# Kernel optimization log

Hardware: AMD Instinct MI355X
Metric: run time of the kernel (lower is better)

## Reference

```python
import jax, jax.numpy as jnp
import numpy as np

B_, L_, D_ = 8, 2048, 1024      # batch, seq_len, d_model
E, DS, K = 2, 16, 4             # expand, d_state, d_conv
DI = E * D_                     # d_inner = 2048
DTR = (D_ + 15) // 16           # dt_rank = 64


def setup_inputs() -> dict:
    key = jax.random.key(0)
    ks = jax.random.split(key, 8)
    g = lambda k, sh, sc=0.02: jax.random.normal(k, sh, jnp.float32) * sc
    return {
        "x": jax.random.normal(ks[0], (B_, L_, D_), jnp.float32),
        "ln_w": jnp.ones((D_,), jnp.float32),
        "ln_b": jnp.zeros((D_,), jnp.float32),
        "W_in": g(ks[1], (D_, 2 * DI)),
        "conv_w": g(ks[2], (DI, 1, K), 0.1),
        "conv_b": jnp.zeros((DI,), jnp.float32),
        "W_x": g(ks[3], (DI, DTR + 2 * DS)),
        "W_dt": g(ks[4], (DTR, DI), 0.1),
        "b_dt": jnp.full((DI,), -4.0, jnp.float32),  # softplus(-4) ~ 0.018 (small init dt)
        "A_log": jnp.log(jnp.broadcast_to(jnp.arange(1, DS + 1, dtype=jnp.float32), (DI, DS))),
        "Dp": jnp.ones((DI,), jnp.float32),
        "W_out": g(ks[5], (DI, D_)),
    }


def _mamba_block(x, ln_w, ln_b, W_in, conv_w, conv_b, W_x, W_dt, b_dt, A_log, Dp, W_out):
    # pre-norm
    mu = jnp.mean(x, axis=-1, keepdims=True)
    var = jnp.var(x, axis=-1, keepdims=True)
    xn = (x - mu) / jnp.sqrt(var + 1e-5) * ln_w + ln_b

    # input projection -> (u, z), each (B, L, DI)
    xz = jnp.einsum('bld,de->ble', xn, W_in)
    u, z = jnp.split(xz, 2, axis=-1)

    # causal depthwise conv1d along L
    uc = jax.lax.conv_general_dilated(
        u.transpose(0, 2, 1), conv_w, window_strides=(1,), padding=[(K - 1, 0)],
        feature_group_count=DI, dimension_numbers=('NCH', 'OIH', 'NCH'))
    u = jax.nn.silu(uc.transpose(0, 2, 1) + conv_b)

    # input-dependent SSM params
    xd = jnp.einsum('bld,de->ble', u, W_x)          # (B, L, DTR + 2*DS)
    dt = jax.nn.softplus(jnp.einsum('blr,rd->bld', xd[..., :DTR], W_dt) + b_dt)  # (B, L, DI)
    Bm = xd[..., DTR:DTR + DS]                       # (B, L, DS)
    Cm = xd[..., DTR + DS:]                          # (B, L, DS)
    A = -jnp.exp(A_log)                              # (DI, DS)

    # selective scan over time; carry h: (B, DI, DS)
    def step(h, inp):
        dt_t, u_t, B_t, C_t = inp                    # (B,DI),(B,DI),(B,DS),(B,DS)
        dA = jnp.exp(dt_t[..., None] * A)            # (B, DI, DS)
        h = h * dA + (dt_t * u_t)[..., None] * B_t[:, None, :]
        y = jnp.einsum('bds,bs->bd', h, C_t)
        return h, y

    h0 = jnp.zeros((x.shape[0], DI, DS), x.dtype)
    xs = (dt.transpose(1, 0, 2), u.transpose(1, 0, 2), Bm.transpose(1, 0, 2), Cm.transpose(1, 0, 2))
    _, ys = jax.lax.scan(step, h0, xs)               # ys: (L, B, DI)

    y = ys.transpose(1, 0, 2) + u * Dp
    y = y * jax.nn.silu(z)
    # output projection + residual (dropout is identity in eval)
    return jnp.einsum('bld,de->ble', y, W_out) + x


def reference(x, ln_w, ln_b, W_in, conv_w, conv_b, W_x, W_dt, b_dt, A_log, Dp, W_out):
    return _mamba_block(x, ln_w, ln_b, W_in, conv_w, conv_b, W_x, W_dt, b_dt, A_log, Dp, W_out)
```

## Files before the change

### kernel.cpp

```cpp
#include <hip/hip_runtime.h>

#define NB 8
#define NL 2048
#define ND 1024
#define NDI 2048
#define NDS 16
#define NDTR 64
#define NM (NB * NL)
#define CH 16
#define CL (NL / CH)

__device__ __forceinline__ float bf2f(unsigned int u) {
  union { unsigned int i; float f; } c; c.i = u << 16; return c.f;
}
__device__ __forceinline__ float lo16(unsigned int w) { return __uint_as_float(w << 16); }
__device__ __forceinline__ float hi16(unsigned int w) { return __uint_as_float(w & 0xffff0000u); }
__device__ __forceinline__ unsigned short f2bf(float f) {
  unsigned int x = __float_as_uint(f);
  x = x + 0x7fffu + ((x >> 16) & 1u);
  return (unsigned short)(x >> 16);
}
__device__ __forceinline__ void dec8(int4 raw, float* f) {
  f[0] = lo16((unsigned)raw.x); f[1] = hi16((unsigned)raw.x);
  f[2] = lo16((unsigned)raw.y); f[3] = hi16((unsigned)raw.y);
  f[4] = lo16((unsigned)raw.z); f[5] = hi16((unsigned)raw.z);
  f[6] = lo16((unsigned)raw.w); f[7] = hi16((unsigned)raw.w);
}
__device__ __forceinline__ float softplus_fast(float x) {
  return fmaxf(x, 0.f) + __logf(1.f + __expf(-fabsf(x)));
}

typedef __bf16 bf16x8 __attribute__((ext_vector_type(8)));
typedef float f32x4 __attribute__((ext_vector_type(4)));

__device__ __forceinline__ void gld_lds16(const unsigned short* g, unsigned short* l) {
  __builtin_amdgcn_global_load_lds(
      (const __attribute__((address_space(1))) unsigned int*)g,
      (__attribute__((address_space(3))) unsigned int*)l, 16, 0, 0);
}

__global__ __launch_bounds__(256) void k_ln(const float* __restrict__ x,
    const float* __restrict__ lw, const float* __restrict__ lb,
    unsigned short* __restrict__ xn)
{
  const int row = blockIdx.x;
  const int tid = threadIdx.x;
  const float* xr = x + (size_t)row * ND;
  float4 v = reinterpret_cast<const float4*>(xr)[tid];
  float s  = v.x + v.y + v.z + v.w;
  float s2 = v.x*v.x + v.y*v.y + v.z*v.z + v.w*v.w;
  #pragma unroll
  for (int m = 32; m >= 1; m >>= 1) {
    s  += __shfl_xor(s, m);
    s2 += __shfl_xor(s2, m);
  }
  __shared__ float red[8];
  const int wid = tid >> 6;
  if ((tid & 63) == 0) { red[wid] = s; red[4 + wid] = s2; }
  __syncthreads();
  s  = red[0] + red[1] + red[2] + red[3];
  s2 = red[4] + red[5] + red[6] + red[7];
  const float mu   = s * (1.0f / ND);
  const float var  = s2 * (1.0f / ND) - mu * mu;
  const float rstd = rsqrtf(var + 1e-5f);
  const float4 wv = reinterpret_cast<const float4*>(lw)[tid];
  const float4 bv = reinterpret_cast<const float4*>(lb)[tid];
  ushort4 o;
  o.x = f2bf((v.x - mu) * rstd * wv.x + bv.x);
  o.y = f2bf((v.y - mu) * rstd * wv.y + bv.y);
  o.z = f2bf((v.z - mu) * rstd * wv.z + bv.z);
  o.w = f2bf((v.w - mu) * rstd * wv.w + bv.w);
  reinterpret_cast<ushort4*>(xn + (size_t)row * ND)[tid] = o;
}

__global__ __launch_bounds__(256) void k_transpose(
    const float* __restrict__ W, unsigned short* __restrict__ WT,
    const int K, const int N)
{
  __shared__ float t[32][33];
  const int k0 = blockIdx.y * 32, n0 = blockIdx.x * 32;
  const int tx = threadIdx.x & 31, ty = threadIdx.x >> 5;
  #pragma unroll
  for (int r = 0; r < 4; ++r)
    t[ty + r * 8][tx] = W[(size_t)(k0 + ty + r * 8) * N + n0 + tx];
  __syncthreads();
  #pragma unroll
  for (int r = 0; r < 4; ++r)
    WT[(size_t)(n0 + ty + r * 8) * K + k0 + tx] = f2bf(t[tx][ty + r * 8]);
}

template<int MODE>
__global__ __launch_bounds__(512, 4) void k_mfma3(
    const unsigned short* __restrict__ A, const unsigned short* __restrict__ BT,
    const int K, const int N, void* __restrict__ O0, void* __restrict__ O1,
    const float* __restrict__ aux)
{
  __shared__ __align__(16) unsigned short sh[24576];
  const int tid = threadIdx.x, lane = tid & 63, wv = tid >> 6;
  const int wm = wv >> 2, wn = wv & 3;
  const int m16 = lane & 15, kb = lane >> 4;
  const int swzs = (((kb * 16) ^ (((m16 >> 1) & 3) << 4)) >> 1);
  const int arow = wm * 64 + m16;
  const int brow = wn * 64 + m16;

  int wg = blockIdx.x;
  const int cpx = gridDim.x >> 3;
  wg = (wg & 7) * cpx + (wg >> 3);
  const int gnx = N >> 8;
  const int m0 = (wg / gnx) << 7;
  const int n0 = (wg % gnx) << 8;

  f32x4 acc[4][4];
  #pragma unroll
  for (int i = 0; i < 4; ++i)
    #pragma unroll
    for (int j = 0; j < 4; ++j)
      #pragma unroll
      for (int r = 0; r < 4; ++r) acc[i][j][r] = 0.f;

  auto STAGE_A = [&](int kg, unsigned short* base) {
    const int s = wv * 64 + lane;
    const int row = s >> 2;
    const int c = (s & 3) ^ ((row >> 1) & 3);
    gld_lds16(A + (size_t)(m0 + row) * K + kg + c * 8, base + wv * 512);
  };
  auto STAGE_B = [&](int kg, unsigned short* base) {
    #pragma unroll
    for (int jj = 0; jj < 2; ++jj) {
      const int s = (wv * 2 + jj) * 64 + lane;
      const int row = s >> 2;
      const int c = (s & 3) ^ ((row >> 1) & 3);
      gld_lds16(BT + (size_t)(n0 + row) * K + kg + c * 8, base + (wv * 2 + jj) * 512);
    }
  };

  STAGE_A(0, sh);
  STAGE_B(0, sh + 4096);
  asm volatile("s_waitcnt vmcnt(0)" ::: "memory");
  __builtin_amdgcn_s_barrier();

  const int NT = K >> 5;
  for (int t = 0; t < NT; ++t) {
    const int buf = t & 1;
    const unsigned short* cA = sh + buf * 12288;
    const unsigned short* cB = cA + 4096;
    unsigned short* nBuf = sh + (buf ^ 1) * 12288;
    const bool more = (t + 1 < NT);
    if (more) {
      const int kn = (t + 1) << 5;
      STAGE_A(kn, nBuf);
      STAGE_B(kn, nBuf + 4096);
    }
    bf16x8 aF[4], bF[4];
    #pragma unroll
    for (int i = 0; i < 4; ++i)
      aF[i] = *reinterpret_cast<const bf16x8*>(cA + (arow + i * 16) * 32 + swzs);
    #pragma unroll
    for (int j = 0; j < 4; ++j)
      bF[j] = *reinterpret_cast<const bf16x8*>(cB + (brow + j * 16) * 32 + swzs);
    __builtin_amdgcn_sched_barrier(0);
    __builtin_amdgcn_s_setprio(1);
    #pragma unroll
    for (int i = 0; i < 4; ++i)
      #pragma unroll
      for (int j = 0; j < 4; ++j)
        acc[i][j] = __builtin_amdgcn_mfma_f32_16x16x32_bf16(aF[i], bF[j], acc[i][j], 0, 0, 0);
    __builtin_amdgcn_s_setprio(0);
    if (more) asm volatile("s_waitcnt vmcnt(0)" ::: "memory");
    __builtin_amdgcn_s_barrier();
  }

  {
    float* fsh = (float*)sh;
    constexpr int LDP = 260;
    const int erow = tid >> 4;
    const int ec0  = tid & 15;
    #pragma unroll
    for (int i = 0; i < 4; ++i) {
      __builtin_amdgcn_s_barrier();
      #pragma unroll
      for (int j = 0; j < 4; ++j)
        #pragma unroll
        for (int r = 0; r < 4; ++r)
          fsh[(wm * 16 + kb * 4 + r) * LDP + wn * 64 + j * 16 + m16] = acc[i][j][r];
      __builtin_amdgcn_s_barrier();
      const int grow = m0 + (erow >> 4) * 64 + i * 16 + (erow & 15);
      #pragma unroll
      for (int q = 0; q < 4; ++q) {
        const int c = (ec0 + q * 16) * 4;
        float4 v = *reinterpret_cast<const float4*>(&fsh[erow * LDP + c]);
        const int colg = n0 + c;
        if constexpr (MODE == 0) {
          ushort4 o = {f2bf(v.x), f2bf(v.y), f2bf(v.z), f2bf(v.w)};
          unsigned short* dst = (colg < NDI)
              ? (unsigned short*)O0 + (size_t)grow * NDI + colg
              : (unsigned short*)O1 + (size_t)grow * NDI + colg - NDI;
          *reinterpret_cast<ushort4*>(dst) = o;
        } else {
          float4 rv = *reinterpret_cast<const float4*>(aux + (size_t)grow * N + colg);
          float4 o = {v.x + rv.x, v.y + rv.y, v.z + rv.z, v.w + rv.w};
          *reinterpret_cast<float4*>((float*)O0 + (size_t)grow * N + colg) = o;
        }
      }
    }
  }
  (void)O1; (void)aux;
}

__global__ __launch_bounds__(256) void k_mfma_dt(
    const unsigned short* __restrict__ A, const unsigned short* __restrict__ BT,
    const int K, void* __restrict__ O0, const float* __restrict__ aux, const int N)
{
  __shared__ __align__(16) unsigned short As[128 * 32];
  __shared__ __align__(16) unsigned short Bs[128 * 32];
  __shared__ __align__(16) float fshd[32 * 132];
  const int tid = threadIdx.x;
  const int lane = tid & 63;
  const int wv = tid >> 6;
  const int wm = wv >> 1, wn = wv & 1;
  const int m0 = blockIdx.y * 128, n0 = blockIdx.x * 128;
  const int m16 = lane & 15, kb = lane >> 4;
  const int wbase = wv * 64;

  f32x4 acc[4][4];
  #pragma unroll
  for (int i = 0; i < 4; ++i)
    #pragma unroll
    for (int j = 0; j < 4; ++j)
      #pragma unroll
      for (int r = 0; r < 4; ++r) acc[i][j][r] = 0.f;

  for (int k0 = 0; k0 < K; k0 += 32) {
    #pragma unroll
    for (int it = 0; it < 2; ++it) {
      const int c = it * 256 + tid;
      const int r = c >> 2, cb = c & 3;
      gld_lds16(A  + (size_t)(m0 + r) * K + k0 + cb * 8, As + (size_t)(it * 256 + wbase) * 8);
      gld_lds16(BT + (size_t)(n0 + r) * K + k0 + cb * 8, Bs + (size_t)(it * 256 + wbase) * 8);
    }
    __syncthreads();
    bf16x8 af[4], bfr[4];
    #pragma unroll
    for (int i = 0; i < 4; ++i)
      af[i] = *reinterpret_cast<const bf16x8*>(&As[(wm * 64 + i * 16 + m16) * 32 + kb * 8]);
    #pragma unroll
    for (int j = 0; j < 4; ++j)
      bfr[j] = *reinterpret_cast<const bf16x8*>(&Bs[(wn * 64 + j * 16 + m16) * 32 + kb * 8]);
    #pragma unroll
    for (int i = 0; i < 4; ++i)
      #pragma unroll
      for (int j = 0; j < 4; ++j)
        acc[i][j] = __builtin_amdgcn_mfma_f32_16x16x32_bf16(af[i], bfr[j], acc[i][j], 0, 0, 0);
    __syncthreads();
  }

  {
    constexpr int LDP = 132;
    const int erow = tid >> 3;
    const int ec0  = tid & 7;
    #pragma unroll
    for (int i = 0; i < 4; ++i) {
      __syncthreads();
      #pragma unroll
      for (int j = 0; j < 4; ++j)
        #pragma unroll
        for (int r = 0; r < 4; ++r)
          fshd[(wm * 16 + kb * 4 + r) * LDP + wn * 64 + j * 16 + m16] = acc[i][j][r];
      __syncthreads();
      const int grow = m0 + (erow >> 4) * 64 + i * 16 + (erow & 15);
      #pragma unroll
      for (int q = 0; q < 4; ++q) {
        const int c = (ec0 + q * 8) * 4;
        float4 v = *reinterpret_cast<const float4*>(&fshd[erow * LDP + c]);
        const int colg = n0 + c;
        ushort4 o;
        o.x = f2bf(softplus_fast(v.x + aux[colg + 0]));
        o.y = f2bf(softplus_fast(v.y + aux[colg + 1]));
        o.z = f2bf(softplus_fast(v.z + aux[colg + 2]));
        o.w = f2bf(softplus_fast(v.w + aux[colg + 3]));
        *reinterpret_cast<ushort4*>((unsigned short*)O0 + (size_t)grow * N + colg) = o;
      }
    }
  }
}

__global__ __launch_bounds__(256) void k_conv(
    const unsigned short* __restrict__ up, const float* __restrict__ cw,
    const float* __restrict__ cb, unsigned short* __restrict__ u)
{
  const int tid = threadIdx.x;
  const int c0 = tid * 8;
  const int lt = blockIdx.x & 127;
  const int b  = blockIdx.x >> 7;
  const int l0 = lt * 16;

  float4 wv[8];
  #pragma unroll
  for (int j = 0; j < 8; ++j)
    wv[j] = reinterpret_cast<const float4*>(cw + (size_t)c0 * 4)[j];
  float bias[8];
  {
    float4 b0 = reinterpret_cast<const float4*>(cb + c0)[0];
    float4 b1 = reinterpret_cast<const float4*>(cb + c0)[1];
    bias[0]=b0.x; bias[1]=b0.y; bias[2]=b0.z; bias[3]=b0.w;
    bias[4]=b1.x; bias[5]=b1.y; bias[6]=b1.z; bias[7]=b1.w;
  }

  const size_t base = ((size_t)b * NL + l0) * NDI + c0;
  float w0[8], w1[8], w2[8];
  if (l0 >= 3) {
    int4 r0 = *reinterpret_cast<const int4*>(up + base - 3 * NDI);
    int4 r1 = *reinterpret_cast<const int4*>(up + base - 2 * NDI);
    int4 r2 = *reinterpret_cast<const int4*>(up + base - 1 * NDI);
    dec8(r0, w0); dec8(r1, w1); dec8(r2, w2);
  } else {
    #pragma unroll
    for (int j = 0; j < 8; ++j) { w0[j] = 0.f; w1[j] = 0.f; w2[j] = 0.f; }
  }

  #pragma unroll
  for (int l = 0; l < 16; ++l) {
    int4 raw = *reinterpret_cast<const int4*>(up + base + (size_t)l * NDI);
    float cur[8];
    dec8(raw, cur);
    unsigned short o[8];
    #pragma unroll
    for (int j = 0; j < 8; ++j) {
      const float a = bias[j] + wv[j].x * w0[j] + wv[j].y * w1[j]
                              + wv[j].z * w2[j] + wv[j].w * cur[j];
      o[j] = f2bf(a / (1.f + __expf(-a)));
    }
    ushort4 o0 = {o[0], o[1], o[2], o[3]};
    ushort4 o1 = {o[4], o[5], o[6], o[7]};
    unsigned short* dst = u + base + (size_t)l * NDI;
    *reinterpret_cast<ushort4*>(dst)     = o0;
    *reinterpret_cast<ushort4*>(dst + 4) = o1;
    #pragma unroll
    for (int j = 0; j < 8; ++j) { w0[j] = w1[j]; w1[j] = w2[j]; w2[j] = cur[j]; }
  }
}

__global__ __launch_bounds__(256) void k_xd_mfma(
    const unsigned short* __restrict__ A, const unsigned short* __restrict__ BT,
    unsigned short* __restrict__ xdt, float* __restrict__ xb,
    float* __restrict__ xc)
{
  __shared__ __align__(16) unsigned short As[2][64 * 32];
  __shared__ __align__(16) unsigned short Bs[2][96 * 32];
  const int tid = threadIdx.x, lane = tid & 63, wvv = tid >> 6;
  const int m0 = blockIdx.x * 64;
  const int m16 = lane & 15, kb = lane >> 4;
  const int sw = (kb ^ ((m16 >> 1) & 3)) * 8;

  f32x4 acc[6];
  #pragma unroll
  for (int j = 0; j < 6; ++j)
    #pragma unroll
    for (int r = 0; r < 4; ++r) acc[j][r] = 0.f;

  auto STG = [&](int bb, int kg) {
    {
      const int row = tid >> 2, c = tid & 3;
      const int sc = c ^ ((row >> 1) & 3);
      gld_lds16(A + (size_t)(m0 + row) * NDI + kg + sc * 8, &As[bb][tid * 8]);
      gld_lds16(BT + (size_t)row * NDI + kg + sc * 8, &Bs[bb][tid * 8]);
    }
    if (tid < 128) {
      const int s = 256 + tid;
      const int row = s >> 2, c = s & 3;
      const int sc = c ^ ((row >> 1) & 3);
      gld_lds16(BT + (size_t)row * NDI + kg + sc * 8, &Bs[bb][s * 8]);
    }
  };

  STG(0, 0);
  asm volatile("s_waitcnt vmcnt(0)" ::: "memory");
  __syncthreads();

  for (int t = 0; t < NDI / 32; ++t) {
    const int cur = t & 1;
    if (t + 1 < NDI / 32) STG(cur ^ 1, (t + 1) * 32);
    bf16x8 af = *reinterpret_cast<const bf16x8*>(&As[cur][(wvv * 16 + m16) * 32 + sw]);
    bf16x8 bfr[6];
    #pragma unroll
    for (int j = 0; j < 6; ++j)
      bfr[j] = *reinterpret_cast<const bf16x8*>(&Bs[cur][(j * 16 + m16) * 32 + sw]);
    #pragma unroll
    for (int j = 0; j < 6; ++j)
      acc[j] = __builtin_amdgcn_mfma_f32_16x16x32_bf16(af, bfr[j], acc[j], 0, 0, 0);
    asm volatile("s_waitcnt vmcnt(0)" ::: "memory");
    __syncthreads();
  }

  const int r0 = kb * 4;
  #pragma unroll
  for (int j = 0; j < 6; ++j) {
    const int col = j * 16 + m16;
    #pragma unroll
    for (int r = 0; r < 4; ++r) {
      const int row = m0 + wvv * 16 + r0 + r;
      const float v = acc[j][r];
      if (j < 4)       xdt[(size_t)row * 64 + col] = f2bf(v);
      else if (j == 4) xb[(size_t)row * 16 + col - 64] = v;
      else             xc[(size_t)row * 16 + col - 80] = v;
    }
  }
}

template<int PHASE>
__global__ __launch_bounds__(256) void k_scan3(
    const unsigned short* __restrict__ dt, unsigned short* __restrict__ u_io,
    const unsigned short* __restrict__ z,
    const float* __restrict__ xb, const float* __restrict__ xc,
    const float* __restrict__ A_log, const float* __restrict__ Dp,
    float* __restrict__ HF, float* __restrict__ Sdt)
{
  const int tid = threadIdx.x;
  const int blk = blockIdx.x;
  const int b = blk >> 7;
  const int c = (blk >> 3) & (CH - 1);
  if (PHASE == 0 && c == CH - 1) return;
  const int d = (blk & 7) * 256 + tid;

  __shared__ float Bsl[CL][16];
  __shared__ float Csl[(PHASE == 1) ? CL : 1][16];
  const size_t rbase = (size_t)b * NL + (size_t)c * CL;
  #pragma unroll
  for (int i = 0; i < 2; ++i) {
    const int idx = i * 256 + tid;
    const int r = idx >> 2, q = idx & 3;
    reinterpret_cast<float4*>(&Bsl[r][q * 4])[0] =
        reinterpret_cast<const float4*>(xb + (rbase + r) * 16)[q];
    if constexpr (PHASE == 1)
      reinterpret_cast<float4*>(&Csl[r][q * 4])[0] =
          reinterpret_cast<const float4*>(xc + (rbase + r) * 16)[q];
  }
  __syncthreads();

  float Ac[16];
  #pragma unroll
  for (int q = 0; q < 4; ++q) {
    float4 a = reinterpret_cast<const float4*>(A_log + (size_t)d * 16)[q];
    Ac[q*4+0] = -__expf(a.x); Ac[q*4+1] = -__expf(a.y);
    Ac[q*4+2] = -__expf(a.z); Ac[q*4+3] = -__expf(a.w);
  }
  bool fastok = true;
  #pragma unroll
  for (int s = 1; s < 16; ++s)
    fastok = fastok && (fabsf(Ac[s] - Ac[0] * (float)(s + 1)) <= 1e-5f * fabsf(Ac[s]));
  const bool fast = __all(fastok);

  const size_t hoff = ((size_t)(b * CH + c) * NDI + d) * 16;
  float h[16];
  if constexpr (PHASE == 0) {
    #pragma unroll
    for (int s = 0; s < 16; ++s) h[s] = 0.f;
  } else {
    #pragma unroll
    for (int q = 0; q < 4; ++q) {
      float4 hv = reinterpret_cast<const float4*>(HF + hoff)[q];
      h[q*4+0] = hv.x; h[q*4+1] = hv.y; h[q*4+2] = hv.z; h[q*4+3] = hv.w;
    }
  }
  const float Dd = Dp[d];
  const float Ac0 = Ac[0];
  float sdt = 0.f;
  size_t idx = rbase * NDI + d;

  if (fast) {
    for (int l = 0; l < CL; ++l, idx += NDI) {
      const float dtv = bf2f(dt[idx]);
      const float uv  = bf2f(u_io[idx]);
      const float dtu = dtv * uv;
      const float qq = __expf(dtv * Ac0);
      float e = qq;
      if constexpr (PHASE == 0) {
        sdt += dtv;
        #pragma unroll
        for (int s = 0; s < 16; ++s) {
          h[s] = h[s] * e + dtu * Bsl[l][s];
          e *= qq;
        }
      } else {
        float yp = 0.f;
        #pragma unroll
        for (int s = 0; s < 16; ++s) {
          h[s] = h[s] * e + dtu * Bsl[l][s];
          yp += h[s] * Csl[l][s];
          e *= qq;
        }
        const float zv = bf2f(z[idx]);
        const float sil = zv / (1.f + __expf(-zv));
        u_io[idx] = f2bf((yp + uv * Dd) * sil);
      }
    }
  } else {
    for (int l = 0; l < CL; ++l, idx += NDI) {
      const float dtv = bf2f(dt[idx]);
      const float uv  = bf2f(u_io[idx]);
      const float dtu = dtv * uv;
      if constexpr (PHASE == 0) {
        sdt += dtv;
        #pragma unroll
        for (int s = 0; s < 16; ++s) {
          const float e = __expf(dtv * Ac[s]);
          h[s] = h[s] * e + dtu * Bsl[l][s];
        }
      } else {
        float yp = 0.f;
        #pragma unroll
        for (int s = 0; s < 16; ++s) {
          const float e = __expf(dtv * Ac[s]);
          h[s] = h[s] * e + dtu * Bsl[l][s];
          yp += h[s] * Csl[l][s];
        }
        const float zv = bf2f(z[idx]);
        const float sil = zv / (1.f + __expf(-zv));
        u_io[idx] = f2bf((yp + uv * Dd) * sil);
      }
    }
  }

  if constexpr (PHASE == 0) {
    #pragma unroll
    for (int q = 0; q < 4; ++q) {
      float4 hv = {h[q*4+0], h[q*4+1], h[q*4+2], h[q*4+3]};
      reinterpret_cast<float4*>(HF + hoff)[q] = hv;
    }
    Sdt[(size_t)(b * CH + c) * NDI + d] = sdt;
  }
}

__global__ __launch_bounds__(256) void k_comb(
    float* __restrict__ HF, const float* __restrict__ Sdt,
    const float* __restrict__ A_log)
{
  const int t = blockIdx.x * 256 + threadIdx.x;
  const int b = t >> 15;
  const int q = t & 32767;
  const int d = q >> 4;
  const float Ac = -__expf(A_log[q]);
  float H = 0.f;
  #pragma unroll
  for (int c = 0; c < CH; ++c) {
    const size_t off = (((size_t)(b * CH + c) * NDI) << 4) + q;
    const float hf = HF[off];
    const float p  = __expf(Ac * Sdt[(size_t)(b * CH + c) * NDI + d]);
    HF[off] = H;
    H = p * H + hf;
  }
}

extern "C" void kernel_launch(void* const* d_in, const int* in_sizes, int n_in,
                              void* d_out, int out_size, void* d_ws, size_t ws_size,
                              hipStream_t stream) {
  (void)in_sizes; (void)n_in; (void)out_size; (void)ws_size;
  const float* x      = (const float*)d_in[0];
  const float* ln_w   = (const float*)d_in[1];
  const float* ln_b   = (const float*)d_in[2];
  const float* W_in   = (const float*)d_in[3];
  const float* conv_w = (const float*)d_in[4];
  const float* conv_b = (const float*)d_in[5];
  const float* W_x    = (const float*)d_in[6];
  const float* W_dt   = (const float*)d_in[7];
  const float* b_dt   = (const float*)d_in[8];
  const float* A_log  = (const float*)d_in[9];
  const float* Dp     = (const float*)d_in[10];
  const float* W_out  = (const float*)d_in[11];
  float* out = (float*)d_out;

  char* ws = (char*)d_ws;
  unsigned short* xn   = (unsigned short*)(ws);
  float*          HF   = (float*)(ws);
  unsigned short* upre = (unsigned short*)(ws + 33554432);
  unsigned short* zbuf = (unsigned short*)(ws + 100663296);
  unsigned short* ubuf = (unsigned short*)(ws + 167772160);
  unsigned short* xdt  = (unsigned short*)(ws + 234881024);
  float*          Sdt  = (float*)(ws + 234881024);
  float*          xb   = (float*)(ws + 236978176);
  float*          xc   = (float*)(ws + 238026752);
  unsigned short* WxT  = (unsigned short*)(ws + 239075328);
  unsigned short* WdtT = (unsigned short*)(ws + 239468544);
  unsigned short* WinT = (unsigned short*)(ws + 240123904);
  unsigned short* WoutT= (unsigned short*)(ws + 248512512);

  dim3 gt1(4096 / 32, 1024 / 32);
  k_transpose<<<gt1, 256, 0, stream>>>(W_in, WinT, 1024, 4096);
  dim3 gt2(1024 / 32, 2048 / 32);
  k_transpose<<<gt2, 256, 0, stream>>>(W_out, WoutT, 2048, 1024);
  dim3 gt3(96 / 32, 2048 / 32);
  k_transpose<<<gt3, 256, 0, stream>>>(W_x, WxT, 2048, 96);
  dim3 gt4(2048 / 32, 64 / 32);
  k_transpose<<<gt4, 256, 0, stream>>>(W_dt, WdtT, 64, 2048);

  k_ln<<<NM, 256, 0, stream>>>(x, ln_w, ln_b, xn);

  k_mfma3<0><<<(NM / 128) * (4096 / 256), 512, 0, stream>>>(
      xn, WinT, 1024, 4096, upre, zbuf, nullptr);

  k_conv<<<NB * (NL / 16), 256, 0, stream>>>(upre, conv_w, conv_b, ubuf);

  k_xd_mfma<<<NM / 64, 256, 0, stream>>>(ubuf, WxT, xdt, xb, xc);

  dim3 g3(2048 / 128, NM / 128);
  k_mfma_dt<<<g3, 256, 0, stream>>>(xdt, WdtT, 64, upre, b_dt, 2048);

  const int nscan = NB * CH * (NDI / 256);
  k_scan3<0><<<nscan, 256, 0, stream>>>(upre, ubuf, zbuf, xb, xc, A_log, Dp, HF, Sdt);
  k_comb<<<NB * NDI * NDS / 256, 256, 0, stream>>>(HF, Sdt, A_log);
  k_scan3<1><<<nscan, 256, 0, stream>>>(upre, ubuf, zbuf, xb, xc, A_log, Dp, HF, Sdt);

  k_mfma3<1><<<(NM / 128) * (1024 / 256), 512, 0, stream>>>(
      ubuf, WoutT, 2048, 1024, out, nullptr, x);
}
```

Before: 550.4 us.

## Enlarge GEMM tile to 256x256 with triple-buffered LDS pipeline

The projection GEMM kernel's block tile grows from 128x256 to 256x256, so each wave computes an 8x4 grid of MFMA tiles and the A and B tiles are reused more. LDS staging changes from double to triple buffering, with global loads issued three K-steps ahead and graded vmcnt waits. This aims to raise arithmetic intensity and hide global load latency for the input and output projections. In exchange it doubles LDS use and accumulator registers, lowers occupancy (launch bounds 2) and halves the number of blocks, which may leave some compute units idle on the smaller output GEMM.

```diff
diff --git a/kernel.cpp b/kernel.cpp
--- a/kernel.cpp
+++ b/kernel.cpp
@@ -90,83 +90,79 @@
 }
 
 template<int MODE>
-__global__ __launch_bounds__(512, 4) void k_mfma3(
+__global__ __launch_bounds__(512, 2) void k_mfma4(
     const unsigned short* __restrict__ A, const unsigned short* __restrict__ BT,
     const int K, const int N, void* __restrict__ O0, void* __restrict__ O1,
     const float* __restrict__ aux)
 {
-  __shared__ __align__(16) unsigned short sh[24576];
+  __shared__ __align__(16) unsigned short sh[49152];
   const int tid = threadIdx.x, lane = tid & 63, wv = tid >> 6;
   const int wm = wv >> 2, wn = wv & 3;
   const int m16 = lane & 15, kb = lane >> 4;
-  const int swzs = (((kb * 16) ^ (((m16 >> 1) & 3) << 4)) >> 1);
-  const int arow = wm * 64 + m16;
-  const int brow = wn * 64 + m16;
+  const int swzs = (kb ^ ((m16 >> 1) & 3)) * 8;
 
   int wg = blockIdx.x;
   const int cpx = gridDim.x >> 3;
   wg = (wg & 7) * cpx + (wg >> 3);
   const int gnx = N >> 8;
-  const int m0 = (wg / gnx) << 7;
+  const int m0 = (wg / gnx) << 8;
   const int n0 = (wg % gnx) << 8;
 
-  f32x4 acc[4][4];
-  #pragma unroll
-  for (int i = 0; i < 4; ++i)
+  f32x4 acc[8][4];
+  #pragma unroll
+  for (int i = 0; i < 8; ++i)
     #pragma unroll
     for (int j = 0; j < 4; ++j)
       #pragma unroll
       for (int r = 0; r < 4; ++r) acc[i][j][r] = 0.f;
 
-  auto STAGE_A = [&](int kg, unsigned short* base) {
-    const int s = wv * 64 + lane;
-    const int row = s >> 2;
-    const int c = (s & 3) ^ ((row >> 1) & 3);
-    gld_lds16(A + (size_t)(m0 + row) * K + kg + c * 8, base + wv * 512);
+  auto STAGE = [&](const unsigned short* X, int x0, int kg, unsigned short* base) {
+    #pragma unroll
+    for (int jj = 0; jj < 2; ++jj) {
+      const int u = jj * 512 + tid;
+      const int row = u >> 2;
+      const int c = (u & 3) ^ ((row >> 1) & 3);
+      gld_lds16(X + (size_t)(x0 + row) * K + kg + c * 8,
+                base + (jj * 512 + wv * 64) * 8);
+    }
   };
-  auto STAGE_B = [&](int kg, unsigned short* base) {
-    #pragma unroll
-    for (int jj = 0; jj < 2; ++jj) {
-      const int s = (wv * 2 + jj) * 64 + lane;
-      const int row = s >> 2;
-      const int c = (s & 3) ^ ((row >> 1) & 3);
-      gld_lds16(BT + (size_t)(n0 + row) * K + kg + c * 8, base + (wv * 2 + jj) * 512);
-    }
+  auto STAGE_T = [&](int kt, int slot) {
+    unsigned short* s = sh + slot * 16384;
+    STAGE(A,  m0, kt * 32, s);
+    STAGE(BT, n0, kt * 32, s + 8192);
   };
 
-  STAGE_A(0, sh);
-  STAGE_B(0, sh + 4096);
-  asm volatile("s_waitcnt vmcnt(0)" ::: "memory");
+  const int NT = K >> 5;
+  STAGE_T(0, 0);
+  STAGE_T(1, 1);
+  STAGE_T(2, 2);
+  asm volatile("s_waitcnt vmcnt(8)" ::: "memory");
   __builtin_amdgcn_s_barrier();
 
-  const int NT = K >> 5;
   for (int t = 0; t < NT; ++t) {
-    const int buf = t & 1;
-    const unsigned short* cA = sh + buf * 12288;
-    const unsigned short* cB = cA + 4096;
-    unsigned short* nBuf = sh + (buf ^ 1) * 12288;
-    const bool more = (t + 1 < NT);
-    if (more) {
-      const int kn = (t + 1) << 5;
-      STAGE_A(kn, nBuf);
-      STAGE_B(kn, nBuf + 4096);
-    }
-    bf16x8 aF[4], bF[4];
-    #pragma unroll
-    for (int i = 0; i < 4; ++i)
-      aF[i] = *reinterpret_cast<const bf16x8*>(cA + (arow + i * 16) * 32 + swzs);
+    const int st = t % 3;
+    const unsigned short* aB = sh + st * 16384;
+    const unsigned short* bB = aB + 8192;
+    bf16x8 aF[8], bF[4];
+    #pragma unroll
+    for (int i = 0; i < 8; ++i)
+      aF[i] = *reinterpret_cast<const bf16x8*>(aB + (wm * 128 + i * 16 + m16) * 32 + swzs);
     #pragma unroll
     for (int j = 0; j < 4; ++j)
-      bF[j] = *reinterpret_cast<const bf16x8*>(cB + (brow + j * 16) * 32 + swzs);
-    __builtin_amdgcn_sched_barrier(0);
+      bF[j] = *reinterpret_cast<const bf16x8*>(bB + (wn * 64 + j * 16 + m16) * 32 + swzs);
     __builtin_amdgcn_s_setprio(1);
     #pragma unroll
-    for (int i = 0; i < 4; ++i)
+    for (int i = 0; i < 8; ++i)
       #pragma unroll
       for (int j = 0; j < 4; ++j)
         acc[i][j] = __builtin_amdgcn_mfma_f32_16x16x32_bf16(aF[i], bF[j], acc[i][j], 0, 0, 0);
     __builtin_amdgcn_s_setprio(0);
-    if (more) asm volatile("s_waitcnt vmcnt(0)" ::: "memory");
+    asm volatile("" ::: "memory");
+    __builtin_amdgcn_s_barrier();
+    if (t + 3 < NT) STAGE_T(t + 3, st);
+    if (t + 3 < NT)      { asm volatile("s_waitcnt vmcnt(8)" ::: "memory"); }
+    else if (t + 2 < NT) { asm volatile("s_waitcnt vmcnt(4)" ::: "memory"); }
+    else if (t + 1 < NT) { asm volatile("s_waitcnt vmcnt(0)" ::: "memory"); }
     __builtin_amdgcn_s_barrier();
   }
 
@@ -176,7 +172,7 @@
     const int erow = tid >> 4;
     const int ec0  = tid & 15;
     #pragma unroll
-    for (int i = 0; i < 4; ++i) {
+    for (int i = 0; i < 8; ++i) {
       __builtin_amdgcn_s_barrier();
       #pragma unroll
       for (int j = 0; j < 4; ++j)
@@ -184,7 +180,7 @@
         for (int r = 0; r < 4; ++r)
           fsh[(wm * 16 + kb * 4 + r) * LDP + wn * 64 + j * 16 + m16] = acc[i][j][r];
       __builtin_amdgcn_s_barrier();
-      const int grow = m0 + (erow >> 4) * 64 + i * 16 + (erow & 15);
+      const int grow = m0 + (erow >> 4) * 128 + i * 16 + (erow & 15);
       #pragma unroll
       for (int q = 0; q < 4; ++q) {
         const int c = (ec0 + q * 16) * 4;
@@ -595,7 +591,7 @@
 
   k_ln<<<NM, 256, 0, stream>>>(x, ln_w, ln_b, xn);
 
-  k_mfma3<0><<<(NM / 128) * (4096 / 256), 512, 0, stream>>>(
+  k_mfma4<0><<<(NM / 256) * (4096 / 256), 512, 0, stream>>>(
       xn, WinT, 1024, 4096, upre, zbuf, nullptr);
 
   k_conv<<<NB * (NL / 16), 256, 0, stream>>>(upre, conv_w, conv_b, ubuf);
@@ -610,6 +606,6 @@
   k_comb<<<NB * NDI * NDS / 256, 256, 0, stream>>>(HF, Sdt, A_log);
   k_scan3<1><<<nscan, 256, 0, stream>>>(upre, ubuf, zbuf, xb, xc, A_log, Dp, HF, Sdt);
 
-  k_mfma3<1><<<(NM / 128) * (1024 / 256), 512, 0, stream>>>(
+  k_mfma4<1><<<(NM / 256) * (1024 / 256), 512, 0, stream>>>(
       ubuf, WoutT, 2048, 1024, out, nullptr, x);
 }
```

New measurement: 554.0 us. Within noise of the previous version (+0.7%).

## Use 256x256 tile GEMM for output projection and fuse weight transposes

Applied to the files above, without the earlier changes.

Adds a 256x256-tile double-buffered MFMA GEMM variant with 8x4 accumulator fragments per wave and uses it for the output projection with residual add. It also merges the four weight transpose launches into one kernel that dispatches on block index. The larger tile raises operand reuse per LDS load and the merged launch cuts per-launch overhead. In exchange, register pressure rises, occupancy drops to two blocks per CU, and the grid shrinks to 256 blocks, roughly one wave of blocks.

```diff
diff --git a/kernel.cpp b/kernel.cpp
--- a/kernel.cpp
+++ b/kernel.cpp
@@ -73,12 +73,21 @@
   reinterpret_cast<ushort4*>(xn + (size_t)row * ND)[tid] = o;
 }
 
-__global__ __launch_bounds__(256) void k_transpose(
-    const float* __restrict__ W, unsigned short* __restrict__ WT,
-    const int K, const int N)
-{
+__global__ __launch_bounds__(256) void k_prep(
+    const float* __restrict__ Wi, const float* __restrict__ Wo,
+    const float* __restrict__ Wx, const float* __restrict__ Wd,
+    unsigned short* __restrict__ WiT, unsigned short* __restrict__ WoT,
+    unsigned short* __restrict__ WxT, unsigned short* __restrict__ WdT)
+{
+  const int bid = blockIdx.x;
+  const float* W; unsigned short* WT; int K, N, local;
+  if (bid < 4096)      { W = Wi; WT = WiT; K = 1024; N = 4096; local = bid; }
+  else if (bid < 6144) { W = Wo; WT = WoT; K = 2048; N = 1024; local = bid - 4096; }
+  else if (bid < 6336) { W = Wx; WT = WxT; K = 2048; N = 96;   local = bid - 6144; }
+  else                 { W = Wd; WT = WdT; K = 64;   N = 2048; local = bid - 6336; }
+  const int gx = N / 32;
+  const int k0 = (local / gx) * 32, n0 = (local % gx) * 32;
   __shared__ float t[32][33];
-  const int k0 = blockIdx.y * 32, n0 = blockIdx.x * 32;
   const int tx = threadIdx.x & 31, ty = threadIdx.x >> 5;
   #pragma unroll
   for (int r = 0; r < 4; ++r)
@@ -87,6 +96,130 @@
   #pragma unroll
   for (int r = 0; r < 4; ++r)
     WT[(size_t)(n0 + ty + r * 8) * K + k0 + tx] = f2bf(t[tx][ty + r * 8]);
+}
+
+template<int MODE>
+__global__ __launch_bounds__(512, 2) void k_mfma2(
+    const unsigned short* __restrict__ A, const unsigned short* __restrict__ BT,
+    const int K, const int N, void* __restrict__ O0, void* __restrict__ O1,
+    const float* __restrict__ aux)
+{
+  __shared__ __align__(16) unsigned short sh[32768];
+  const int tid = threadIdx.x, lane = tid & 63, wv = tid >> 6;
+  const int wm = wv >> 2, wn = wv & 3;
+  const int m16 = lane & 15, kb = lane >> 4;
+  const int swzs = (((kb * 16) ^ (((m16 >> 1) & 3) << 4)) >> 1);
+  const int arow = wm * 128 + m16;
+  const int brow = wn * 64 + m16;
+
+  int wg = blockIdx.x;
+  const int cpx = gridDim.x >> 3;
+  wg = (wg & 7) * cpx + (wg >> 3);
+  const int gnx = N >> 8;
+  const int m0 = (wg / gnx) << 8;
+  const int n0 = (wg % gnx) << 8;
+
+  f32x4 acc[8][4];
+  #pragma unroll
+  for (int i = 0; i < 8; ++i)
+    #pragma unroll
+    for (int j = 0; j < 4; ++j)
+      #pragma unroll
+      for (int r = 0; r < 4; ++r) acc[i][j][r] = 0.f;
+
+  auto STAGE = [&](const unsigned short* X, int x0, int kg, unsigned short* base) {
+    #pragma unroll
+    for (int jj = 0; jj < 2; ++jj) {
+      const int s = (wv * 2 + jj) * 64 + lane;
+      const int row = s >> 2;
+      const int c = (lane & 3) ^ ((row >> 1) & 3);
+      gld_lds16(X + (size_t)(x0 + row) * K + kg + c * 8, base + (wv * 2 + jj) * 512);
+    }
+  };
+  auto RD_A = [&](bf16x8* dst, const unsigned short* base, int FH) {
+    #pragma unroll
+    for (int i = 0; i < 4; ++i)
+      dst[i] = *reinterpret_cast<const bf16x8*>(base + (arow + FH * 64 + i * 16) * 32 + swzs);
+  };
+  auto RD_B = [&](bf16x8* dst, const unsigned short* base) {
+    #pragma unroll
+    for (int j = 0; j < 4; ++j)
+      dst[j] = *reinterpret_cast<const bf16x8*>(base + (brow + j * 16) * 32 + swzs);
+  };
+  auto MM = [&](const bf16x8* aF, const bf16x8* bF, int off) {
+    #pragma unroll
+    for (int i = 0; i < 4; ++i)
+      #pragma unroll
+      for (int j = 0; j < 4; ++j)
+        acc[off + i][j] = __builtin_amdgcn_mfma_f32_16x16x32_bf16(aF[i], bF[j], acc[off + i][j], 0, 0, 0);
+  };
+
+  STAGE(A,  m0, 0, sh);
+  STAGE(BT, n0, 0, sh + 8192);
+  asm volatile("s_waitcnt vmcnt(0)" ::: "memory");
+  __builtin_amdgcn_s_barrier();
+
+  const int NT = K >> 5;
+  for (int t = 0; t < NT; ++t) {
+    const int buf = t & 1;
+    const unsigned short* cA = sh + buf * 16384;
+    const unsigned short* cB = cA + 8192;
+    unsigned short* nA = sh + (buf ^ 1) * 16384;
+    const bool more = (t + 1 < NT);
+    if (more) {
+      const int kn = (t + 1) << 5;
+      STAGE(A,  m0, kn, nA);
+      STAGE(BT, n0, kn, nA + 8192);
+    }
+    bf16x8 a0[4], a1[4], bF[4];
+    RD_A(a0, cA, 0);
+    RD_B(bF, cB);
+    RD_A(a1, cA, 1);
+    __builtin_amdgcn_sched_barrier(0);
+    __builtin_amdgcn_s_setprio(1);
+    MM(a0, bF, 0);
+    MM(a1, bF, 4);
+    __builtin_amdgcn_s_setprio(0);
+    if (more) asm volatile("s_waitcnt vmcnt(0)" ::: "memory");
+    __builtin_amdgcn_s_barrier();
+  }
+
+  {
+    float* fsh = (float*)sh;
+    constexpr int LDP = 260;
+    const int erow = tid >> 4;
+    const int ec0  = tid & 15;
+    const int growb = m0 + (erow >> 4) * 128 + (erow & 15);
+    #pragma unroll
+    for (int i = 0; i < 8; ++i) {
+      __builtin_amdgcn_s_barrier();
+      #pragma unroll
+      for (int j = 0; j < 4; ++j)
+        #pragma unroll
+        for (int r = 0; r < 4; ++r)
+          fsh[(wm * 16 + kb * 4 + r) * LDP + wn * 64 + j * 16 + m16] = acc[i][j][r];
+      __builtin_amdgcn_s_barrier();
+      const int grow = growb + i * 16;
+      #pragma unroll
+      for (int q = 0; q < 4; ++q) {
+        const int c = (ec0 + q * 16) * 4;
+        float4 v = *reinterpret_cast<const float4*>(&fsh[erow * LDP + c]);
+        const int colg = n0 + c;
+        if constexpr (MODE == 0) {
+          ushort4 o = {f2bf(v.x), f2bf(v.y), f2bf(v.z), f2bf(v.w)};
+          unsigned short* dst = (colg < NDI)
+              ? (unsigned short*)O0 + (size_t)grow * NDI + colg
+              : (unsigned short*)O1 + (size_t)grow * NDI + colg - NDI;
+          *reinterpret_cast<ushort4*>(dst) = o;
+        } else {
+          float4 rv = *reinterpret_cast<const float4*>(aux + (size_t)grow * N + colg);
+          float4 o = {v.x + rv.x, v.y + rv.y, v.z + rv.z, v.w + rv.w};
+          *reinterpret_cast<float4*>((float*)O0 + (size_t)grow * N + colg) = o;
+        }
+      }
+    }
+  }
+  (void)O1; (void)aux;
 }
 
 template<int MODE>
@@ -584,14 +717,7 @@
   unsigned short* WinT = (unsigned short*)(ws + 240123904);
   unsigned short* WoutT= (unsigned short*)(ws + 248512512);
 
-  dim3 gt1(4096 / 32, 1024 / 32);
-  k_transpose<<<gt1, 256, 0, stream>>>(W_in, WinT, 1024, 4096);
-  dim3 gt2(1024 / 32, 2048 / 32);
-  k_transpose<<<gt2, 256, 0, stream>>>(W_out, WoutT, 2048, 1024);
-  dim3 gt3(96 / 32, 2048 / 32);
-  k_transpose<<<gt3, 256, 0, stream>>>(W_x, WxT, 2048, 96);
-  dim3 gt4(2048 / 32, 64 / 32);
-  k_transpose<<<gt4, 256, 0, stream>>>(W_dt, WdtT, 64, 2048);
+  k_prep<<<6464, 256, 0, stream>>>(W_in, W_out, W_x, W_dt, WinT, WoutT, WxT, WdtT);
 
   k_ln<<<NM, 256, 0, stream>>>(x, ln_w, ln_b, xn);
 
@@ -610,6 +736,6 @@
   k_comb<<<NB * NDI * NDS / 256, 256, 0, stream>>>(HF, Sdt, A_log);
   k_scan3<1><<<nscan, 256, 0, stream>>>(upre, ubuf, zbuf, xb, xc, A_log, Dp, HF, Sdt);
 
-  k_mfma3<1><<<(NM / 128) * (1024 / 256), 512, 0, stream>>>(
+  k_mfma2<1><<<(NM / 256) * (1024 / 256), 512, 0, stream>>>(
       ubuf, WoutT, 2048, 1024, out, nullptr, x);
 }
```

Result: no change. 541.1 us, median of 2 (-1.7%).
